# Kernel tuning notes

Measured on AMD Instinct MI355X. Metric: run time of the kernel, lower is better.

The kernel has to match this reference:

```python
import jax, jax.numpy as jnp
import numpy as np

N = 50000   # num nodes
E = 400000  # num edges (avg degree 8)
D = 256     # in_channels
H = 256     # hidden_channels
C = 64      # out_channels
K = 2       # k_hops


def setup_inputs() -> dict:
    key = jax.random.key(0)
    ks = jax.random.split(key, 10)
    x = jax.random.normal(ks[0], (N, D), dtype=jnp.float32)
    edge_index = jax.random.randint(ks[1], (2, E), 0, N, dtype=jnp.int32)
    s = 0.05
    # per-hop linears of the single H2GCNConv (weights stored [in, out])
    W0 = jax.random.normal(ks[2], (D, H), jnp.float32) * s
    W1 = jax.random.normal(ks[3], (D, H), jnp.float32) * s
    W2 = jax.random.normal(ks[4], (D, H), jnp.float32) * s
    b0 = jnp.zeros((H,), jnp.float32)
    b1 = jnp.zeros((H,), jnp.float32)
    b2 = jnp.zeros((H,), jnp.float32)
    # classifier: h2_out_dim = H*(K+1) = 768 -> C
    Wc = jax.random.normal(ks[5], (H * (K + 1), C), jnp.float32) * s
    bc = jnp.zeros((C,), jnp.float32)
    return {"x": x, "edge_index": edge_index, "num_nodes": N,
            "W0": W0, "b0": b0, "W1": W1, "b1": b1, "W2": W2, "b2": b2,
            "Wc": Wc, "bc": bc}


def _normalize_adj(edge_index, num_nodes):
    # add self loops, then D^{-1/2} A D^{-1/2} edge weights
    loops = jnp.arange(num_nodes, dtype=edge_index.dtype)
    ei = jnp.concatenate([edge_index, jnp.stack([loops, loops])], axis=1)
    row, col = ei[0], ei[1]
    deg = jax.ops.segment_sum(jnp.ones(row.shape[0], jnp.float32), row,
                              num_segments=num_nodes)
    dis = jnp.where(deg > 0, deg ** -0.5, 0.0)  # inf -> 0 for isolated nodes
    return ei, dis[row] * dis[col]


def _sparse_mm(edge_index, edge_weight, x, num_nodes):
    # gather -> scale -> scatter-add (COO SpMM)
    row, col = edge_index[0], edge_index[1]
    msg = x[col] * edge_weight[:, None]  # [E', F]
    return jax.ops.segment_sum(msg, row, num_segments=num_nodes)


def reference(x, edge_index, num_nodes, W0, b0, W1, b1, W2, b2, Wc, bc):
    ei, ew = _normalize_adj(edge_index, num_nodes)
    # H2GCNConv: ego + k-hop aggregates, each through its own linear, concat
    outs = [x @ W0 + b0]
    cur = x
    for Wk, bk in ((W1, b1), (W2, b2)):
        cur = _sparse_mm(ei, ew, cur, num_nodes)
        outs.append(cur @ Wk + bk)
    h = jax.nn.relu(jnp.concatenate(outs, axis=1))  # [N, 3H]
    # dropout p=0 / eval mode -> identity
    return h @ Wc + bc
```

## Files before the change

kernel.cpp:

```cpp
#include <hip/hip_runtime.h>


#define FD 256
#define CO 64
#define SB 512

using frag_ab = __attribute__((ext_vector_type(8))) short;
using f32x4   = __attribute__((ext_vector_type(4))) float;
typedef unsigned short u16;
typedef unsigned int   u32;

__device__ __forceinline__ u16 f2bf(float f) {
    u32 u = __builtin_bit_cast(u32, f);
    return (u16)((u + 0x7FFFu + ((u >> 16) & 1u)) >> 16);
}
__device__ __forceinline__ float bfl(u32 packed) {
    return __builtin_bit_cast(float, packed << 16);
}
__device__ __forceinline__ float bfh(u32 packed) {
    return __builtin_bit_cast(float, packed & 0xFFFF0000u);
}

__device__ __forceinline__ void gll16(const void* g, void* l) {
    __builtin_amdgcn_global_load_lds(
        (const __attribute__((address_space(1))) u32*)g,
        (__attribute__((address_space(3))) u32*)l, 16, 0, 0);
}

#define BAR()  __builtin_amdgcn_s_barrier()
#define WLG0() asm volatile("s_waitcnt lgkmcnt(0)" ::: "memory")
#define WVM0() asm volatile("s_waitcnt vmcnt(0)" ::: "memory")
#define WVM2() asm volatile("s_waitcnt vmcnt(2)" ::: "memory")

__global__ void zerok(int4* __restrict__ deg4, int4* __restrict__ fill4, int n4) {
    int i = blockIdx.x * blockDim.x + threadIdx.x;
    int4 z = make_int4(0, 0, 0, 0);
    if (i < n4) { deg4[i] = z; fill4[i] = z; }
}
__global__ void count_kernel(const int* __restrict__ ei0, int* deg, int e) {
    int i = blockIdx.x * blockDim.x + threadIdx.x;
    if (i < e) atomicAdd(&deg[ei0[i]], 1);
}
__global__ void scan1(const int* __restrict__ deg, int* __restrict__ rowptr,
                      int* __restrict__ bsum, float* __restrict__ dis, int n) {
    __shared__ int sh[SB];
    int tid = threadIdx.x;
    int i = blockIdx.x * SB + tid;
    int v = (i < n) ? deg[i] + 1 : 0;
    if (i < n) dis[i] = rsqrtf((float)v);
    sh[tid] = v;
    __syncthreads();
    for (int off = 1; off < SB; off <<= 1) {
        int add = (tid >= off) ? sh[tid - off] : 0;
        __syncthreads();
        sh[tid] += add;
        __syncthreads();
    }
    if (i < n) rowptr[i] = sh[tid] - v;
    if (tid == SB - 1) bsum[blockIdx.x] = sh[tid];
}
__global__ void scan2(const int* __restrict__ bsum, int* __restrict__ bscan, int nb) {
    __shared__ int sh[128];
    int tid = threadIdx.x;
    int v = (tid < nb) ? bsum[tid] : 0;
    sh[tid] = v;
    __syncthreads();
    for (int off = 1; off < 128; off <<= 1) {
        int add = (tid >= off) ? sh[tid - off] : 0;
        __syncthreads();
        sh[tid] += add;
        __syncthreads();
    }
    if (tid < nb) bscan[tid] = sh[tid] - v;
    if (tid == nb - 1) bscan[nb] = sh[tid];
}
__global__ void scan3(int* rowptr, const int* __restrict__ bscan, int n, int nb) {
    int i = blockIdx.x * 256 + threadIdx.x;
    if (i < n) rowptr[i] += bscan[i / SB];
    if (i == n) rowptr[n] = bscan[nb];
}
__global__ void fill_kernel(const int* __restrict__ ei, const float* __restrict__ dis,
                            const int* __restrict__ rowptr, int* fill,
                            int2* __restrict__ cw, int e, int n) {
    int i = blockIdx.x * blockDim.x + threadIdx.x;
    if (i >= e + n) return;
    int r, c;
    if (i < e) { r = ei[i]; c = ei[e + i]; }
    else       { r = i - e; c = r; }
    float w = dis[r] * dis[c];
    int pos = rowptr[r] + atomicAdd(&fill[r], 1);
    int2 p; p.x = c; p.y = __float_as_int(w);
    cw[pos] = p;
}

__global__ void conv_kernel(const float* __restrict__ x, u16* __restrict__ xb, int total4) {
    int i = blockIdx.x * blockDim.x + threadIdx.x;
    if (i < total4) {
        float4 v = ((const float4*)x)[i];
        ushort4 o;
        o.x = f2bf(v.x); o.y = f2bf(v.y); o.z = f2bf(v.z); o.w = f2bf(v.w);
        ((ushort4*)xb)[i] = o;
    }
}
__global__ void wtrans_kernel(const float* __restrict__ W0, const float* __restrict__ W1,
                              const float* __restrict__ W2, const float* __restrict__ Wc,
                              u16* __restrict__ WkT, u16* __restrict__ WcT) {
    __shared__ u16 tl[64][65];
    int b = blockIdx.x;
    const float* src; u16* dst; int R, C, r0, c0;
    if (b < 48) {
        int k = b >> 4, t = b & 15;
        src = (k == 0) ? W0 : (k == 1) ? W1 : W2;
        dst = WkT + k * 65536;
        R = 256; C = 256; r0 = (t >> 2) * 64; c0 = (t & 3) * 64;
    } else {
        int t = b - 48;
        src = Wc; dst = WcT;
        R = 768; C = 64; r0 = t * 64; c0 = 0;
    }
    int tid = threadIdx.x;
    int rr = tid >> 4, cc = (tid & 15) * 4;
    #pragma unroll
    for (int it = 0; it < 4; ++it) {
        int r = it * 16 + rr;
        float4 v = *(const float4*)(src + (size_t)(r0 + r) * C + c0 + cc);
        tl[cc + 0][r] = f2bf(v.x); tl[cc + 1][r] = f2bf(v.y);
        tl[cc + 2][r] = f2bf(v.z); tl[cc + 3][r] = f2bf(v.w);
    }
    __syncthreads();
    #pragma unroll
    for (int it = 0; it < 4; ++it) {
        int crow = it * 16 + rr;
        ushort4 o;
        o.x = tl[crow][cc + 0]; o.y = tl[crow][cc + 1];
        o.z = tl[crow][cc + 2]; o.w = tl[crow][cc + 3];
        *(ushort4*)(dst + (size_t)(c0 + crow) * R + r0 + cc) = o;
    }
}

__global__ void spmm_bf16(const int* __restrict__ rowptr, const int2* __restrict__ cw,
                          const u16* __restrict__ xb, u16* __restrict__ outb, int n) {
    int tid = threadIdx.x;
    int lane = tid & 63;
    int row = blockIdx.x * 8 + ((tid >> 6) << 1) + (lane >> 5);
    if (row >= n) return;
    int l32 = lane & 31;
    int p0 = rowptr[row], p1 = rowptr[row + 1];
    float a[8];
    #pragma unroll
    for (int j = 0; j < 8; ++j) a[j] = 0.f;

    for (int p = p0; p < p1; p += 8) {
        int2 cwv[8]; uint4 v[8];
        #pragma unroll
        for (int u = 0; u < 8; ++u) {
            int q = p + u;
            bool ok = q < p1;
            cwv[u] = cw[ok ? q : p0];
            if (!ok) cwv[u].y = 0;
        }
        #pragma unroll
        for (int u = 0; u < 8; ++u)
            v[u] = *(const uint4*)(xb + (size_t)cwv[u].x * FD + l32 * 8);
        #pragma unroll
        for (int u = 0; u < 8; ++u) {
            float wt = __int_as_float(cwv[u].y);
            a[0] += wt * bfl(v[u].x); a[1] += wt * bfh(v[u].x);
            a[2] += wt * bfl(v[u].y); a[3] += wt * bfh(v[u].y);
            a[4] += wt * bfl(v[u].z); a[5] += wt * bfh(v[u].z);
            a[6] += wt * bfl(v[u].w); a[7] += wt * bfh(v[u].w);
        }
    }
    uint4 o;
    o.x = (u32)f2bf(a[0]) | ((u32)f2bf(a[1]) << 16);
    o.y = (u32)f2bf(a[2]) | ((u32)f2bf(a[3]) << 16);
    o.z = (u32)f2bf(a[4]) | ((u32)f2bf(a[5]) << 16);
    o.w = (u32)f2bf(a[6]) | ((u32)f2bf(a[7]) << 16);
    *(uint4*)(outb + (size_t)row * FD + l32 * 8) = o;
}

__launch_bounds__(256, 2)
__global__ void fused_gemm(const u16* __restrict__ xb, const u16* __restrict__ agg1b,
                           const u16* __restrict__ agg2b, const u16* __restrict__ WkT,
                           const float* __restrict__ b0, const float* __restrict__ b1,
                           const float* __restrict__ b2, const u16* __restrict__ WcT,
                           const float* __restrict__ bc, float* __restrict__ out, int n) {
    __shared__ __align__(16) char lds[73728];
    char* Tl = lds + 40960;

    const int tid = threadIdx.x;
    const int w = tid >> 6, l = tid & 63;
    const int l4 = l >> 4, lm = l & 15;
    const int row0 = blockIdx.x * 64;
    const int rr = w * 16 + lm;

    f32x4 oacc[4];
    #pragma unroll
    for (int am = 0; am < 4; ++am) oacc[am] = (f32x4)(0.f);

    for (int seg = 0; seg < 3; ++seg) {
        const u16* inb = (seg == 0) ? xb : (seg == 1) ? agg1b : agg2b;
        const u16* WT  = WkT + (size_t)seg * 65536;
        const float* bk = (seg == 0) ? b0 : (seg == 1) ? b1 : b2;

        auto stageB = [&](int kt, int pb) {
            {
                int L = tid * 16;
                int r = L >> 6, s = (L >> 4) & 3;
                int gr = row0 + r; if (gr > n - 1) gr = n - 1;
                gll16(inb + (size_t)gr * FD + kt * 32 + (s ^ (r & 3)) * 8,
                      lds + pb * 4096 + L);
            }
            #pragma unroll
            for (int i = 0; i < 4; ++i) {
                int L = tid * 16 + i * 4096;
                int j = L >> 6, s = (L >> 4) & 3;
                gll16(WT + (size_t)j * FD + kt * 32 + (s ^ (j & 3)) * 8,
                      lds + 8192 + pb * 16384 + L);
            }
        };

        f32x4 acc[4][4];
        #pragma unroll
        for (int jm = 0; jm < 4; ++jm)
            #pragma unroll
            for (int rn = 0; rn < 4; ++rn) acc[jm][rn] = (f32x4)(0.f);

        stageB(0, 0);
        WVM0();
        BAR();

        #pragma unroll
        for (int kt = 0; kt < 8; ++kt) {
            char* curA = lds + (kt & 1) * 4096;
            char* curW = lds + 8192 + (kt & 1) * 16384;
            if (kt < 7) stageB(kt + 1, (kt + 1) & 1);

            frag_ab af[4], bf_[4];
            #pragma unroll
            for (int jm = 0; jm < 4; ++jm) {
                int j = w * 64 + jm * 16 + lm;
                af[jm] = *(const frag_ab*)(curW + j * 64 + ((l4 ^ (j & 3)) << 4));
            }
            #pragma unroll
            for (int rn = 0; rn < 4; ++rn) {
                int r = rn * 16 + lm;
                bf_[rn] = *(const frag_ab*)(curA + r * 64 + ((l4 ^ (r & 3)) << 4));
            }
            #pragma unroll
            for (int jm = 0; jm < 4; ++jm)
                #pragma unroll
                for (int rn = 0; rn < 4; ++rn)
                    acc[jm][rn] = __builtin_amdgcn_mfma_f32_16x16x32_bf16(af[jm], bf_[rn], acc[jm][rn], 0, 0, 0);

            if (kt < 7) WVM0();
            WLG0();
            BAR();
        }

        auto stageC = [&](int kt2, int pb) {
            #pragma unroll
            for (int i = 0; i < 2; ++i) {
                int L = tid * 16 + i * 4096;
                int c = L >> 7, s = (L >> 4) & 7;
                gll16(WcT + (size_t)c * 768 + seg * 256 + kt2 * 64 + (s ^ (c & 7)) * 8,
                      lds + 8192 + pb * 8192 + L);
            }
        };
        stageC(0, 0);

        #pragma unroll
        for (int jm = 0; jm < 4; ++jm) {
            int j0 = w * 64 + jm * 16 + l4 * 4;
            float4 bb = *(const float4*)(bk + j0);
            #pragma unroll
            for (int rn = 0; rn < 4; ++rn) {
                int r = rn * 16 + lm;
                f32x4 v = acc[jm][rn];
                ushort4 p;
                p.x = f2bf(fmaxf(v[0] + bb.x, 0.f));
                p.y = f2bf(fmaxf(v[1] + bb.y, 0.f));
                p.z = f2bf(fmaxf(v[2] + bb.z, 0.f));
                p.w = f2bf(fmaxf(v[3] + bb.w, 0.f));
                *(ushort4*)(Tl + r * 512 + (((j0 >> 3) ^ (r & 7)) << 4) + (j0 & 7) * 2) = p;
            }
        }
        WLG0();
        BAR();

        #pragma unroll
        for (int kt2 = 0; kt2 < 4; ++kt2) {
            char* cw_ = lds + 8192 + (kt2 & 1) * 8192;
            if (kt2 < 3) {
                stageC(kt2 + 1, (kt2 + 1) & 1);
                WVM2();
            } else {
                WVM0();
            }
            BAR();
            #pragma unroll
            for (int kk2 = 0; kk2 < 2; ++kk2) {
                int g = kt2 * 8 + kk2 * 4 + l4;
                frag_ab bfr = *(const frag_ab*)(Tl + rr * 512 + ((g ^ (rr & 7)) << 4));
                #pragma unroll
                for (int am = 0; am < 4; ++am) {
                    int c = am * 16 + lm;
                    frag_ab afr = *(const frag_ab*)(cw_ + c * 128 + (((kk2 * 4 + l4) ^ (c & 7)) << 4));
                    oacc[am] = __builtin_amdgcn_mfma_f32_16x16x32_bf16(afr, bfr, oacc[am], 0, 0, 0);
                }
            }
            WLG0();
            BAR();
        }
    }

    int gr = row0 + rr;
    if (gr < n) {
        #pragma unroll
        for (int am = 0; am < 4; ++am) {
            float4 bb = *(const float4*)(bc + am * 16 + l4 * 4);
            float4 o;
            o.x = oacc[am][0] + bb.x;
            o.y = oacc[am][1] + bb.y;
            o.z = oacc[am][2] + bb.z;
            o.w = oacc[am][3] + bb.w;
            *(float4*)(out + (size_t)gr * CO + am * 16 + l4 * 4) = o;
        }
    }
}

extern "C" void kernel_launch(void* const* d_in, const int* in_sizes, int n_in,
                              void* d_out, int out_size, void* d_ws, size_t ws_size,
                              hipStream_t stream) {
    const float* x  = (const float*)d_in[0];
    const int*   ei = (const int*)d_in[1];
    const float* W0 = (const float*)d_in[3];
    const float* b0 = (const float*)d_in[4];
    const float* W1 = (const float*)d_in[5];
    const float* b1 = (const float*)d_in[6];
    const float* W2 = (const float*)d_in[7];
    const float* b2 = (const float*)d_in[8];
    const float* Wc = (const float*)d_in[9];
    const float* bc = (const float*)d_in[10];
    float* out = (float*)d_out;

    const int n  = in_sizes[0] / FD;
    const int e  = in_sizes[1] / 2;
    const int ep = e + n;
    const int nb = (n + SB - 1) / SB;

    char* ws = (char*)d_ws;
    size_t o = 0;
    auto take = [&](size_t nbytes) -> char* {
        char* p = ws + o;
        o += (nbytes + 255) & ~(size_t)255;
        return p;
    };
    int*   deg    = (int*)  take((size_t)n * 4);
    int*   fill   = (int*)  take((size_t)n * 4);
    float* dis    = (float*)take((size_t)n * 4);
    int*   rowptr = (int*)  take((size_t)(n + 1) * 4);
    int*   bsum   = (int*)  take((size_t)(nb + 1) * 4);
    int*   bscan  = (int*)  take((size_t)(nb + 1) * 4);
    int2*  cw     = (int2*) take((size_t)ep * 8);
    u16*   xb     = (u16*)  take((size_t)n * FD * 2);
    u16*   agg1b  = (u16*)  take((size_t)n * FD * 2);
    u16*   agg2b  = (u16*)  take((size_t)n * FD * 2);
    u16*   WkT    = (u16*)  take((size_t)3 * FD * FD * 2);
    u16*   WcT    = (u16*)  take((size_t)CO * 3 * FD * 2);
    (void)ws_size; (void)n_in; (void)out_size;

    const int n4 = (n + 3) / 4;
    zerok       <<<(n4 + 255) / 256, 256, 0, stream>>>((int4*)deg, (int4*)fill, n4);
    count_kernel<<<(e + 255) / 256, 256, 0, stream>>>(ei, deg, e);
    scan1       <<<nb, SB, 0, stream>>>(deg, rowptr, bsum, dis, n);
    scan2       <<<1, 128, 0, stream>>>(bsum, bscan, nb);
    scan3       <<<(n + 256) / 256, 256, 0, stream>>>(rowptr, bscan, n, nb);
    fill_kernel <<<(ep + 255) / 256, 256, 0, stream>>>(ei, dis, rowptr, fill, cw, e, n);

    const int total4 = n * FD / 4;
    conv_kernel  <<<(total4 + 255) / 256, 256, 0, stream>>>(x, xb, total4);
    wtrans_kernel<<<60, 256, 0, stream>>>(W0, W1, W2, Wc, WkT, WcT);

    spmm_bf16<<<(n + 7) / 8, 256, 0, stream>>>(rowptr, cw, xb, agg1b, n);
    spmm_bf16<<<(n + 7) / 8, 256, 0, stream>>>(rowptr, cw, agg1b, agg2b, n);

    fused_gemm<<<(n + 63) / 64, 256, 0, stream>>>(xb, agg1b, agg2b, WkT,
                                                  b0, b1, b2, WcT, bc, out, n);
}
```

Before: 194.0 us.

## Read classifier weights directly from global to shrink LDS and raise occupancy

Drops the double-buffered LDS staging of the classifier weight tile (WcT). The classifier MFMA loop now loads its A fragments straight from global memory (WcT is small and should stay cached) and no longer needs barriers per k-step. This cuts LDS from 72KB to 40KB, and launch bounds are raised to allow 4 blocks per CU. In exchange, each wave issues uncoalesced-ish global loads inside the MFMA loop with no prefetch, which can expose latency. Register pressure also rises under the tighter launch bounds.

New measurement: 240.7 us. +24.1%, slower.

```diff
diff --git a/kernel.cpp b/kernel.cpp
--- a/kernel.cpp
+++ b/kernel.cpp
@@ -30,7 +30,6 @@
 #define BAR()  __builtin_amdgcn_s_barrier()
 #define WLG0() asm volatile("s_waitcnt lgkmcnt(0)" ::: "memory")
 #define WVM0() asm volatile("s_waitcnt vmcnt(0)" ::: "memory")
-#define WVM2() asm volatile("s_waitcnt vmcnt(2)" ::: "memory")
 
 __global__ void zerok(int4* __restrict__ deg4, int4* __restrict__ fill4, int n4) {
     int i = blockIdx.x * blockDim.x + threadIdx.x;
@@ -179,14 +178,14 @@
     *(uint4*)(outb + (size_t)row * FD + l32 * 8) = o;
 }
 
-__launch_bounds__(256, 2)
+__launch_bounds__(256, 4)
 __global__ void fused_gemm(const u16* __restrict__ xb, const u16* __restrict__ agg1b,
                            const u16* __restrict__ agg2b, const u16* __restrict__ WkT,
                            const float* __restrict__ b0, const float* __restrict__ b1,
                            const float* __restrict__ b2, const u16* __restrict__ WcT,
                            const float* __restrict__ bc, float* __restrict__ out, int n) {
-    __shared__ __align__(16) char lds[73728];
-    char* Tl = lds + 40960;
+    __shared__ __align__(16) char lds[40960];
+    char* Tl = lds + 8192;
 
     const int tid = threadIdx.x;
     const int w = tid >> 6, l = tid & 63;
@@ -257,17 +256,6 @@
             WLG0();
             BAR();
         }
-
-        auto stageC = [&](int kt2, int pb) {
-            #pragma unroll
-            for (int i = 0; i < 2; ++i) {
-                int L = tid * 16 + i * 4096;
-                int c = L >> 7, s = (L >> 4) & 7;
-                gll16(WcT + (size_t)c * 768 + seg * 256 + kt2 * 64 + (s ^ (c & 7)) * 8,
-                      lds + 8192 + pb * 8192 + L);
-            }
-        };
-        stageC(0, 0);
 
         #pragma unroll
         for (int jm = 0; jm < 4; ++jm) {
@@ -289,29 +277,17 @@
         BAR();
 
         #pragma unroll
-        for (int kt2 = 0; kt2 < 4; ++kt2) {
-            char* cw_ = lds + 8192 + (kt2 & 1) * 8192;
-            if (kt2 < 3) {
-                stageC(kt2 + 1, (kt2 + 1) & 1);
-                WVM2();
-            } else {
-                WVM0();
-            }
-            BAR();
-            #pragma unroll
-            for (int kk2 = 0; kk2 < 2; ++kk2) {
-                int g = kt2 * 8 + kk2 * 4 + l4;
-                frag_ab bfr = *(const frag_ab*)(Tl + rr * 512 + ((g ^ (rr & 7)) << 4));
-                #pragma unroll
-                for (int am = 0; am < 4; ++am) {
-                    int c = am * 16 + lm;
-                    frag_ab afr = *(const frag_ab*)(cw_ + c * 128 + (((kk2 * 4 + l4) ^ (c & 7)) << 4));
-                    oacc[am] = __builtin_amdgcn_mfma_f32_16x16x32_bf16(afr, bfr, oacc[am], 0, 0, 0);
-                }
-            }
-            WLG0();
-            BAR();
-        }
+        for (int ks = 0; ks < 8; ++ks) {
+            frag_ab tb = *(const frag_ab*)(Tl + rr * 512 + (((ks * 4 + l4) ^ (rr & 7)) << 4));
+            #pragma unroll
+            for (int am = 0; am < 4; ++am) {
+                int c = am * 16 + lm;
+                frag_ab afr = *(const frag_ab*)(WcT + (size_t)c * 768 + seg * 256 + ks * 32 + l4 * 8);
+                oacc[am] = __builtin_amdgcn_mfma_f32_16x16x32_bf16(afr, tb, oacc[am], 0, 0, 0);
+            }
+        }
+        WLG0();
+        BAR();
     }
 
     int gr = row0 + rr;
```
